# Kernel optimization log

Hardware: AMD Instinct MI355X
Metric: run time of the kernel (lower is better)

Reference implementation:

```python
import jax, jax.numpy as jnp
import numpy as np

C = 256
C8 = C // 8


def setup_inputs() -> dict:
    key = jax.random.key(0)
    ks = jax.random.split(key, 9)
    B, H, W = 4, 64, 64
    x1 = jax.random.normal(ks[0], (B, C, H, W), dtype=jnp.float32)
    x2 = jax.random.normal(ks[1], (B, C, H, W), dtype=jnp.float32)
    s = 1.0 / np.sqrt(C)
    Wq = jax.random.normal(ks[2], (C8, C), dtype=jnp.float32) * s
    bq = jax.random.normal(ks[3], (C8,), dtype=jnp.float32) * s
    Wk = jax.random.normal(ks[4], (C8, C), dtype=jnp.float32) * s
    bk = jax.random.normal(ks[5], (C8,), dtype=jnp.float32) * s
    Wv = jax.random.normal(ks[6], (C, C), dtype=jnp.float32) * s
    bv = jax.random.normal(ks[7], (C,), dtype=jnp.float32) * s
    gamma = jax.random.normal(ks[8], (1,), dtype=jnp.float32) * 0.1
    return {"x1": x1, "x2": x2, "Wq": Wq, "bq": bq, "Wk": Wk, "bk": bk,
            "Wv": Wv, "bv": bv, "gamma": gamma}


def reference(x1, x2, Wq, bq, Wk, bk, Wv, bv, gamma):
    B, Cc, H, W = x1.shape
    N = H * W
    xf = x1.reshape(B, Cc, N)                     # flatten spatial: B,C,N
    # 1x1 convs are per-position matmuls over channels
    q = jnp.einsum('oc,bcn->bno', Wq, xf) + bq    # B,N,C8 (proj_query permuted)
    k = jnp.einsum('oc,bcn->bon', Wk, xf) + bk[None, :, None]   # B,C8,N
    v = jnp.einsum('oc,bcn->bon', Wv, xf) + bv[None, :, None]   # B,C,N
    energy = jnp.einsum('bnc,bcm->bnm', q, k)     # B,N,N (unscaled)
    attn = jax.nn.softmax(energy, axis=-1)        # softmax over keys
    # out[b,c,m] = sum_n v[b,c,n] * attn[b,m,n]
    out = jnp.einsum('bcn,bmn->bcm', v, attn).reshape(B, Cc, H, W)
    return gamma[0] * out + x1
```

## Files before the change

### kernel.cpp

```cpp
#include <hip/hip_runtime.h>
#include <math.h>

#define CH   256
#define C8K  32
#define NPOS 4096
#define BQ   4

typedef __attribute__((ext_vector_type(8))) short bf16x8;
typedef __attribute__((ext_vector_type(4))) float f32x4;

__device__ __forceinline__ unsigned short f2bf(float f) {
    unsigned int u = __float_as_uint(f);
    u = (u + 0x7FFFu + ((u >> 16) & 1u)) >> 16;
    return (unsigned short)u;
}
__device__ __forceinline__ float bf2f(unsigned int h) {
    return __uint_as_float(h << 16);
}

__global__ void prep_w(const float* __restrict__ Wq, const float* __restrict__ Wk,
                       const float* __restrict__ Wv,
                       unsigned short* __restrict__ Whi, unsigned short* __restrict__ Wlo)
{
    const int idx  = blockIdx.x * 256 + threadIdx.x;
    const int e0   = idx * 4;
    const int row  = e0 >> 8;
    const int col  = e0 & 255;
    const float* src;
    if (row < 32)       src = Wq + row * 256 + col;
    else if (row < 64)  src = Wk + (row - 32) * 256 + col;
    else                src = Wv + (row - 64) * 256 + col;
    const float4 v = *reinterpret_cast<const float4*>(src);
    unsigned short h[4], l[4];
    const float* pv = &v.x;
    #pragma unroll
    for (int i = 0; i < 4; ++i) {
        h[i] = f2bf(pv[i]);
        l[i] = f2bf(pv[i] - bf2f((unsigned int)h[i]));
    }
    uint2 ph, pl;
    ph.x = (unsigned)h[0] | ((unsigned)h[1] << 16);
    ph.y = (unsigned)h[2] | ((unsigned)h[3] << 16);
    pl.x = (unsigned)l[0] | ((unsigned)l[1] << 16);
    pl.y = (unsigned)l[2] | ((unsigned)l[3] << 16);
    *reinterpret_cast<uint2*>(Whi + e0) = ph;
    *reinterpret_cast<uint2*>(Wlo + e0) = pl;
}

__global__ __launch_bounds__(512, 1) void proj_kernel(
    const float* __restrict__ x1,
    const unsigned short* __restrict__ Whi, const unsigned short* __restrict__ Wlo,
    const float* __restrict__ bq, const float* __restrict__ bk,
    const float* __restrict__ bv,
    unsigned short* __restrict__ Qhi, unsigned short* __restrict__ Qlo,
    unsigned short* __restrict__ Khi, unsigned short* __restrict__ Klo,
    unsigned short* __restrict__ Vw)
{
    __shared__ __align__(16) unsigned short xh[64 * 136];
    __shared__ __align__(16) unsigned short xl[64 * 136];

    const int t      = threadIdx.x;
    const int l      = t & 63;
    const int w      = t >> 6;
    const int ns     = w & 3;
    const int rh     = w >> 2;
    const int lane15 = l & 15;
    const int g      = l >> 4;
    const int b      = blockIdx.y;
    const int n0     = blockIdx.x * 64;
    const int ncol   = n0 + ns * 16 + lane15;

    const int nq = t & 15, c0 = t >> 4;

    f32x4 acc[10];
    #pragma unroll
    for (int rtl = 0; rtl < 10; ++rtl) acc[rtl] = (f32x4){0.f, 0.f, 0.f, 0.f};

    for (int h = 0; h < 2; ++h) {
        if (h) __syncthreads();
        #pragma unroll
        for (int i = 0; i < 4; ++i) {
            const int ch = c0 + 32 * i;
            const float4 v = *reinterpret_cast<const float4*>(
                x1 + ((size_t)(b * CH + h * 128 + ch) * NPOS) + n0 + nq * 4);
            #pragma unroll
            for (int r = 0; r < 4; ++r) {
                const int n = nq * 4 + r;
                const float f = (&v.x)[r];
                const unsigned short hi = f2bf(f);
                xh[n * 136 + ch] = hi;
                xl[n * 136 + ch] = f2bf(f - bf2f((unsigned int)hi));
            }
        }
        __syncthreads();

        #pragma unroll
        for (int ks2 = 0; ks2 < 4; ++ks2) {
            const int ks = h * 4 + ks2;
            const bf16x8 bh = *reinterpret_cast<const bf16x8*>(
                xh + (ns * 16 + lane15) * 136 + ks2 * 32 + g * 8);
            const bf16x8 bl = *reinterpret_cast<const bf16x8*>(
                xl + (ns * 16 + lane15) * 136 + ks2 * 32 + g * 8);
            const unsigned short* wh =
                Whi + (size_t)(rh * 160 + lane15) * 256 + ks * 32 + g * 8;
            const unsigned short* wl =
                Wlo + (size_t)(rh * 160 + lane15) * 256 + ks * 32 + g * 8;
            #pragma unroll
            for (int rtl = 0; rtl < 10; ++rtl) {
                const bf16x8 ah = *reinterpret_cast<const bf16x8*>(wh + rtl * 16 * 256);
                const bf16x8 al = *reinterpret_cast<const bf16x8*>(wl + rtl * 16 * 256);
                acc[rtl] = __builtin_amdgcn_mfma_f32_16x16x32_bf16(ah, bh, acc[rtl], 0, 0, 0);
                acc[rtl] = __builtin_amdgcn_mfma_f32_16x16x32_bf16(ah, bl, acc[rtl], 0, 0, 0);
                acc[rtl] = __builtin_amdgcn_mfma_f32_16x16x32_bf16(al, bh, acc[rtl], 0, 0, 0);
            }
        }
    }

    #pragma unroll
    for (int rtl = 0; rtl < 10; ++rtl) {
        const int rt  = rh * 10 + rtl;
        const int ch0 = rt * 16 + g * 4;
        if (rt < 4) {
            const float* bias   = (rt < 2) ? bq : bk;
            unsigned short* dhi = (rt < 2) ? Qhi : Khi;
            unsigned short* dlo = (rt < 2) ? Qlo : Klo;
            const int c0q = ch0 - (rt < 2 ? 0 : 32);
            unsigned short hq[4], lq[4];
            #pragma unroll
            for (int r = 0; r < 4; ++r) {
                const float val = acc[rtl][r] + bias[c0q + r];
                hq[r] = f2bf(val);
                lq[r] = f2bf(val - bf2f((unsigned int)hq[r]));
            }
            const size_t off = ((size_t)b * NPOS + ncol) * C8K + c0q;
            uint2 ph, pl;
            ph.x = (unsigned)hq[0] | ((unsigned)hq[1] << 16);
            ph.y = (unsigned)hq[2] | ((unsigned)hq[3] << 16);
            pl.x = (unsigned)lq[0] | ((unsigned)lq[1] << 16);
            pl.y = (unsigned)lq[2] | ((unsigned)lq[3] << 16);
            *reinterpret_cast<uint2*>(dhi + off) = ph;
            *reinterpret_cast<uint2*>(dlo + off) = pl;
        } else {
            const int cv = ch0 - 64;
            #pragma unroll
            for (int r = 0; r < 4; ++r) {
                const float val = acc[rtl][r] + bv[cv + r];
                Vw[((size_t)b * CH + cv + r) * NPOS + ncol] = f2bf(val);
            }
        }
    }
}

__global__ __launch_bounds__(512, 1) void attn_kernel(
    const unsigned short* __restrict__ Qhi, const unsigned short* __restrict__ Qlo,
    const unsigned short* __restrict__ Khi, const unsigned short* __restrict__ Klo,
    const unsigned short* __restrict__ Vw,  const float* __restrict__ x1,
    const float* __restrict__ gamma, float* __restrict__ out)
{
    __shared__ __align__(16) unsigned char smem[47360];
    float*          smWave = (float*)smem;
    float*          smInv  = (float*)(smem + 1024);
    unsigned short* Vt     = (unsigned short*)(smem + 1280);
    unsigned short* Pt     = (unsigned short*)(smem + 1280 + 36864);
    unsigned short* Ot     = Vt;

    const int t      = threadIdx.x;
    const int l      = t & 63;
    const int w      = t >> 6;
    const int ns     = w & 3;
    const int mh     = w >> 2;
    const int lane15 = l & 15;
    const int g      = l >> 4;

    const int wg   = blockIdx.x;
    const int xcd  = wg & 7;
    const int slot = wg >> 3;
    const int b    = xcd >> 1;
    const int mt   = ((xcd & 1) << 5) + slot;
    const int m0   = mt << 6;

    const size_t qkBase = (size_t)b * NPOS * C8K;

    bf16x8 qh[2], ql[2];
    #pragma unroll
    for (int j = 0; j < 2; ++j) {
        const size_t off = qkBase + (size_t)(m0 + (mh * 2 + j) * 16 + lane15) * C8K + g * 8;
        qh[j] = *reinterpret_cast<const bf16x8*>(Qhi + off);
        ql[j] = *reinterpret_cast<const bf16x8*>(Qlo + off);
    }
    const size_t kOffBase = qkBase + (size_t)(ns * 16 + lane15) * C8K + g * 8;
    bf16x8 kh = *reinterpret_cast<const bf16x8*>(Khi + kOffBase);
    bf16x8 kl = *reinterpret_cast<const bf16x8*>(Klo + kOffBase);

    const int vcq = t >> 3, vng = t & 7;
    const unsigned short* vsrcBase = Vw + (size_t)b * CH * NPOS + vng * 8;

    f32x4 acc[2][4];
    #pragma unroll
    for (int j = 0; j < 2; ++j)
        #pragma unroll
        for (int ct = 0; ct < 4; ++ct)
            acc[j][ct] = (f32x4){0.f, 0.f, 0.f, 0.f};
    float psum[2] = {0.f, 0.f};

    for (int nt = 0; nt < 64; ++nt) {
        const int n0 = nt << 6;
        __syncthreads();

        uint4 vld[4];
        #pragma unroll
        for (int i = 0; i < 4; ++i)
            vld[i] = *reinterpret_cast<const uint4*>(
                vsrcBase + (size_t)(vcq + 64 * i) * NPOS + n0);
        const int nn = (nt < 63) ? (n0 + 64) : n0;
        bf16x8 knh = *reinterpret_cast<const bf16x8*>(Khi + kOffBase + (size_t)nn * C8K);
        bf16x8 knl = *reinterpret_cast<const bf16x8*>(Klo + kOffBase + (size_t)nn * C8K);

        float pe[2][4];
        __builtin_amdgcn_s_setprio(1);
        #pragma unroll
        for (int j = 0; j < 2; ++j) {
            f32x4 s = (f32x4){0.f, 0.f, 0.f, 0.f};
            s = __builtin_amdgcn_mfma_f32_16x16x32_bf16(kh, qh[j], s, 0, 0, 0);
            s = __builtin_amdgcn_mfma_f32_16x16x32_bf16(kh, ql[j], s, 0, 0, 0);
            s = __builtin_amdgcn_mfma_f32_16x16x32_bf16(kl, qh[j], s, 0, 0, 0);
            #pragma unroll
            for (int r = 0; r < 4; ++r) {
                const float e = __expf(s[r]);
                pe[j][r] = e;
                psum[j] += e;
            }
        }
        __builtin_amdgcn_s_setprio(0);
        #pragma unroll
        for (int j = 0; j < 2; ++j) {
            uint2 pk;
            pk.x = (unsigned)f2bf(pe[j][0]) | ((unsigned)f2bf(pe[j][1]) << 16);
            pk.y = (unsigned)f2bf(pe[j][2]) | ((unsigned)f2bf(pe[j][3]) << 16);
            *reinterpret_cast<uint2*>(
                Pt + ((mh * 2 + j) * 16 + lane15) * 72 + ns * 16 + g * 4) = pk;
        }
        #pragma unroll
        for (int i = 0; i < 4; ++i)
            *reinterpret_cast<uint4*>(Vt + (vcq + 64 * i) * 72 + vng * 8) = vld[i];
        __syncthreads();

        __builtin_amdgcn_s_setprio(1);
        #pragma unroll
        for (int ks = 0; ks < 2; ++ks) {
            bf16x8 pa[2], vb[4];
            #pragma unroll
            for (int j = 0; j < 2; ++j)
                pa[j] = *reinterpret_cast<const bf16x8*>(
                    Pt + (mh * 32 + j * 16 + lane15) * 72 + ks * 32 + g * 8);
            #pragma unroll
            for (int ct = 0; ct < 4; ++ct)
                vb[ct] = *reinterpret_cast<const bf16x8*>(
                    Vt + (ns * 64 + ct * 16 + lane15) * 72 + ks * 32 + g * 8);
            #pragma unroll
            for (int j = 0; j < 2; ++j)
                #pragma unroll
                for (int ct = 0; ct < 4; ++ct)
                    acc[j][ct] = __builtin_amdgcn_mfma_f32_16x16x32_bf16(
                        pa[j], vb[ct], acc[j][ct], 0, 0, 0);
        }
        __builtin_amdgcn_s_setprio(0);

        kh = knh; kl = knl;
    }

    #pragma unroll
    for (int j = 0; j < 2; ++j) {
        float v = psum[j];
        v += __shfl_xor(v, 16, 64);
        v += __shfl_xor(v, 32, 64);
        psum[j] = v;
    }
    if (l < 16) {
        #pragma unroll
        for (int j = 0; j < 2; ++j)
            smWave[w * 32 + j * 16 + lane15] = psum[j];
    }
    __syncthreads();
    if (t < 64) {
        const int mh2 = t >> 5, ml = t & 31;
        const float d = smWave[(mh2 * 4 + 0) * 32 + ml] + smWave[(mh2 * 4 + 1) * 32 + ml]
                      + smWave[(mh2 * 4 + 2) * 32 + ml] + smWave[(mh2 * 4 + 3) * 32 + ml];
        smInv[t] = 1.f / d;
    }
    __syncthreads();

    #pragma unroll
    for (int j = 0; j < 2; ++j) {
        const float4 inv4 = *reinterpret_cast<const float4*>(smInv + mh * 32 + j * 16 + g * 4);
        #pragma unroll
        for (int ct = 0; ct < 4; ++ct) {
            const int c = ns * 64 + ct * 16 + lane15;
            const f32x4 a = acc[j][ct];
            uint2 pk;
            pk.x = (unsigned)f2bf(a[0] * inv4.x) | ((unsigned)f2bf(a[1] * inv4.y) << 16);
            pk.y = (unsigned)f2bf(a[2] * inv4.z) | ((unsigned)f2bf(a[3] * inv4.w) << 16);
            *reinterpret_cast<uint2*>(Ot + c * 72 + mh * 32 + j * 16 + g * 4) = pk;
        }
    }
    __syncthreads();

    const float gm = gamma[0];
    {
        const int mq = t & 15, c0 = t >> 4;
        #pragma unroll 4
        for (int i = 0; i < 8; ++i) {
            const int c = c0 + (i << 5);
            const size_t off = ((size_t)(b * CH + c)) * NPOS + m0 + mq * 4;
            const uint2 pk = *reinterpret_cast<const uint2*>(Ot + c * 72 + mq * 4);
            const float4 xv = *reinterpret_cast<const float4*>(x1 + off);
            float4 ov;
            ov.x = gm * bf2f(pk.x & 0xFFFFu)  + xv.x;
            ov.y = gm * bf2f(pk.x >> 16)      + xv.y;
            ov.z = gm * bf2f(pk.y & 0xFFFFu)  + xv.z;
            ov.w = gm * bf2f(pk.y >> 16)      + xv.w;
            *reinterpret_cast<float4*>(out + off) = ov;
        }
    }
}

extern "C" void kernel_launch(void* const* d_in, const int* in_sizes, int n_in,
                              void* d_out, int out_size, void* d_ws, size_t ws_size,
                              hipStream_t stream)
{
    const float* x1    = (const float*)d_in[0];
    const float* Wq    = (const float*)d_in[2];
    const float* bq    = (const float*)d_in[3];
    const float* Wk    = (const float*)d_in[4];
    const float* bk    = (const float*)d_in[5];
    const float* Wv    = (const float*)d_in[6];
    const float* bv    = (const float*)d_in[7];
    const float* gamma = (const float*)d_in[8];
    float* out = (float*)d_out;

    unsigned short* ws  = (unsigned short*)d_ws;
    const size_t QK     = (size_t)BQ * NPOS * C8K;
    unsigned short* Qhi = ws;
    unsigned short* Qlo = ws + QK;
    unsigned short* Khi = ws + 2 * QK;
    unsigned short* Klo = ws + 3 * QK;
    unsigned short* Vw  = ws + 4 * QK;
    unsigned short* Whi = Vw + (size_t)BQ * CH * NPOS;
    unsigned short* Wlo = Whi + 320 * 256;

    prep_w<<<dim3(80), 256, 0, stream>>>(Wq, Wk, Wv, Whi, Wlo);

    proj_kernel<<<dim3(64, BQ), 512, 0, stream>>>(
        x1, Whi, Wlo, bq, bk, bv, Qhi, Qlo, Khi, Klo, Vw);

    attn_kernel<<<dim3(256), 512, 0, stream>>>(
        Qhi, Qlo, Khi, Klo, Vw, x1, gamma, out);
}
```

Baseline: 225.4 us.

## Shrink attention tile to 32 queries and load V fragments directly from global

The attention kernel now uses 256-thread blocks handling 32 query rows each (512 blocks, two per CU) instead of 512-thread blocks handling 64 rows. V tiles are no longer staged through LDS: each wave loads its MFMA B-operand fragments straight from global memory into registers, which removes the V LDS writes, reads and the LDS footprint. In exchange, each V tile is now fetched by twice as many blocks, raising global/L2 traffic for V, and register pressure rises from holding eight V fragments per iteration.

After: 273.5 us. 21.4% more time.

```diff
diff --git a/kernel.cpp b/kernel.cpp
--- a/kernel.cpp
+++ b/kernel.cpp
@@ -151,24 +151,21 @@
     }
 }
 
-__global__ __launch_bounds__(512, 1) void attn_kernel(
+__global__ __launch_bounds__(256, 2) void attn_kernel(
     const unsigned short* __restrict__ Qhi, const unsigned short* __restrict__ Qlo,
     const unsigned short* __restrict__ Khi, const unsigned short* __restrict__ Klo,
     const unsigned short* __restrict__ Vw,  const float* __restrict__ x1,
     const float* __restrict__ gamma, float* __restrict__ out)
 {
-    __shared__ __align__(16) unsigned char smem[47360];
+    __shared__ __align__(16) unsigned char smem[25728];
     float*          smWave = (float*)smem;
-    float*          smInv  = (float*)(smem + 1024);
-    unsigned short* Vt     = (unsigned short*)(smem + 1280);
-    unsigned short* Pt     = (unsigned short*)(smem + 1280 + 36864);
-    unsigned short* Ot     = Vt;
+    float*          smInv  = (float*)(smem + 512);
+    unsigned short* Pt     = (unsigned short*)(smem + 640);
+    unsigned short* Ot     = (unsigned short*)(smem + 5248);
 
     const int t      = threadIdx.x;
     const int l      = t & 63;
-    const int w      = t >> 6;
-    const int ns     = w & 3;
-    const int mh     = w >> 2;
+    const int ns     = t >> 6;
     const int lane15 = l & 15;
     const int g      = l >> 4;
 
@@ -176,15 +173,15 @@
     const int xcd  = wg & 7;
     const int slot = wg >> 3;
     const int b    = xcd >> 1;
-    const int mt   = ((xcd & 1) << 5) + slot;
-    const int m0   = mt << 6;
+    const int mt   = ((xcd & 1) << 6) + slot;
+    const int m0   = mt << 5;
 
     const size_t qkBase = (size_t)b * NPOS * C8K;
 
     bf16x8 qh[2], ql[2];
     #pragma unroll
     for (int j = 0; j < 2; ++j) {
-        const size_t off = qkBase + (size_t)(m0 + (mh * 2 + j) * 16 + lane15) * C8K + g * 8;
+        const size_t off = qkBase + (size_t)(m0 + j * 16 + lane15) * C8K + g * 8;
         qh[j] = *reinterpret_cast<const bf16x8*>(Qhi + off);
         ql[j] = *reinterpret_cast<const bf16x8*>(Qlo + off);
     }
@@ -192,8 +189,8 @@
     bf16x8 kh = *reinterpret_cast<const bf16x8*>(Khi + kOffBase);
     bf16x8 kl = *reinterpret_cast<const bf16x8*>(Klo + kOffBase);
 
-    const int vcq = t >> 3, vng = t & 7;
-    const unsigned short* vsrcBase = Vw + (size_t)b * CH * NPOS + vng * 8;
+    const unsigned short* vBase =
+        Vw + (size_t)b * CH * NPOS + (size_t)(ns * 64 + lane15) * NPOS + g * 8;
 
     f32x4 acc[2][4];
     #pragma unroll
@@ -207,11 +204,13 @@
         const int n0 = nt << 6;
         __syncthreads();
 
-        uint4 vld[4];
-        #pragma unroll
-        for (int i = 0; i < 4; ++i)
-            vld[i] = *reinterpret_cast<const uint4*>(
-                vsrcBase + (size_t)(vcq + 64 * i) * NPOS + n0);
+        bf16x8 vf[8];
+        #pragma unroll
+        for (int ks = 0; ks < 2; ++ks)
+            #pragma unroll
+            for (int ct = 0; ct < 4; ++ct)
+                vf[ks * 4 + ct] = *reinterpret_cast<const bf16x8*>(
+                    vBase + (size_t)(ct * 16) * NPOS + n0 + ks * 32);
         const int nn = (nt < 63) ? (n0 + 64) : n0;
         bf16x8 knh = *reinterpret_cast<const bf16x8*>(Khi + kOffBase + (size_t)nn * C8K);
         bf16x8 knl = *reinterpret_cast<const bf16x8*>(Klo + kOffBase + (size_t)nn * C8K);
@@ -238,31 +237,24 @@
             pk.x = (unsigned)f2bf(pe[j][0]) | ((unsigned)f2bf(pe[j][1]) << 16);
             pk.y = (unsigned)f2bf(pe[j][2]) | ((unsigned)f2bf(pe[j][3]) << 16);
             *reinterpret_cast<uint2*>(
-                Pt + ((mh * 2 + j) * 16 + lane15) * 72 + ns * 16 + g * 4) = pk;
-        }
-        #pragma unroll
-        for (int i = 0; i < 4; ++i)
-            *reinterpret_cast<uint4*>(Vt + (vcq + 64 * i) * 72 + vng * 8) = vld[i];
+                Pt + (j * 16 + lane15) * 72 + ns * 16 + g * 4) = pk;
+        }
         __syncthreads();
 
         __builtin_amdgcn_s_setprio(1);
         #pragma unroll
         for (int ks = 0; ks < 2; ++ks) {
-            bf16x8 pa[2], vb[4];
+            bf16x8 pa[2];
             #pragma unroll
             for (int j = 0; j < 2; ++j)
                 pa[j] = *reinterpret_cast<const bf16x8*>(
-                    Pt + (mh * 32 + j * 16 + lane15) * 72 + ks * 32 + g * 8);
-            #pragma unroll
-            for (int ct = 0; ct < 4; ++ct)
-                vb[ct] = *reinterpret_cast<const bf16x8*>(
-                    Vt + (ns * 64 + ct * 16 + lane15) * 72 + ks * 32 + g * 8);
+                    Pt + (j * 16 + lane15) * 72 + ks * 32 + g * 8);
             #pragma unroll
             for (int j = 0; j < 2; ++j)
                 #pragma unroll
                 for (int ct = 0; ct < 4; ++ct)
                     acc[j][ct] = __builtin_amdgcn_mfma_f32_16x16x32_bf16(
-                        pa[j], vb[ct], acc[j][ct], 0, 0, 0);
+                        pa[j], vf[ks * 4 + ct], acc[j][ct], 0, 0, 0);
         }
         __builtin_amdgcn_s_setprio(0);
 
@@ -279,20 +271,18 @@
     if (l < 16) {
         #pragma unroll
         for (int j = 0; j < 2; ++j)
-            smWave[w * 32 + j * 16 + lane15] = psum[j];
+            smWave[ns * 32 + j * 16 + lane15] = psum[j];
     }
     __syncthreads();
-    if (t < 64) {
-        const int mh2 = t >> 5, ml = t & 31;
-        const float d = smWave[(mh2 * 4 + 0) * 32 + ml] + smWave[(mh2 * 4 + 1) * 32 + ml]
-                      + smWave[(mh2 * 4 + 2) * 32 + ml] + smWave[(mh2 * 4 + 3) * 32 + ml];
+    if (t < 32) {
+        const float d = smWave[t] + smWave[32 + t] + smWave[64 + t] + smWave[96 + t];
         smInv[t] = 1.f / d;
     }
     __syncthreads();
 
     #pragma unroll
     for (int j = 0; j < 2; ++j) {
-        const float4 inv4 = *reinterpret_cast<const float4*>(smInv + mh * 32 + j * 16 + g * 4);
+        const float4 inv4 = *reinterpret_cast<const float4*>(smInv + j * 16 + g * 4);
         #pragma unroll
         for (int ct = 0; ct < 4; ++ct) {
             const int c = ns * 64 + ct * 16 + lane15;
@@ -300,19 +290,19 @@
             uint2 pk;
             pk.x = (unsigned)f2bf(a[0] * inv4.x) | ((unsigned)f2bf(a[1] * inv4.y) << 16);
             pk.y = (unsigned)f2bf(a[2] * inv4.z) | ((unsigned)f2bf(a[3] * inv4.w) << 16);
-            *reinterpret_cast<uint2*>(Ot + c * 72 + mh * 32 + j * 16 + g * 4) = pk;
+            *reinterpret_cast<uint2*>(Ot + c * 40 + j * 16 + g * 4) = pk;
         }
     }
     __syncthreads();
 
     const float gm = gamma[0];
     {
-        const int mq = t & 15, c0 = t >> 4;
+        const int mq = t & 7, c0 = t >> 3;
         #pragma unroll 4
         for (int i = 0; i < 8; ++i) {
             const int c = c0 + (i << 5);
             const size_t off = ((size_t)(b * CH + c)) * NPOS + m0 + mq * 4;
-            const uint2 pk = *reinterpret_cast<const uint2*>(Ot + c * 72 + mq * 4);
+            const uint2 pk = *reinterpret_cast<const uint2*>(Ot + c * 40 + mq * 4);
             const float4 xv = *reinterpret_cast<const float4*>(x1 + off);
             float4 ov;
             ov.x = gm * bf2f(pk.x & 0xFFFFu)  + xv.x;
@@ -353,6 +343,6 @@
     proj_kernel<<<dim3(64, BQ), 512, 0, stream>>>(
         x1, Whi, Wlo, bq, bk, bv, Qhi, Qlo, Khi, Klo, Vw);
 
-    attn_kernel<<<dim3(256), 512, 0, stream>>>(
+    attn_kernel<<<dim3(512), 256, 0, stream>>>(
         Qhi, Qlo, Khi, Klo, Vw, x1, gamma, out);
 }
```
